# Performance work log

Hardware: AMD Instinct MI355X
Metric: run time of the kernel (lower is better)

## Reference

```python
import jax, jax.numpy as jnp
import numpy as np

BETA = 0.25

def setup_inputs() -> dict:
    key = jax.random.key(0)
    k1, k2 = jax.random.split(key)
    z = jax.random.normal(k1, (8, 4096, 256), dtype=jnp.float32)
    emb = jax.random.normal(k2, (8192, 256), dtype=jnp.float32) * (1.0 / 8192.0)
    code_age = jnp.zeros((8192,), dtype=jnp.float32)
    code_usage = jnp.zeros((8192,), dtype=jnp.float32)
    return {"z": z, "emb": emb, "code_age": code_age, "code_usage": code_usage}

def reference(z, emb, code_age, code_usage):
    e_dim = emb.shape[-1]
    z_flat = z.reshape(-1, e_dim)  # [M, d]
    # squared euclidean distance (same argmin as torch.cdist)
    z2 = jnp.sum(z_flat * z_flat, axis=-1, keepdims=True)          # [M, 1]
    e2 = jnp.sum(emb * emb, axis=-1)[None, :]                       # [1, n_e]
    dist = z2 - 2.0 * jnp.einsum('md,nd->mn', z_flat, emb) + e2     # [M, n_e]
    idx = jnp.argmin(dist, axis=1)                                  # [M]
    z_q = emb[idx].reshape(z.shape)                                 # gather
    # losses (forward values; stop_gradients irrelevant for fwd)
    diff2 = (z_q - z) ** 2
    loss_commit = BETA * jnp.mean(diff2)   # beta * mean((sg(z_q) - z)^2)
    loss_codebook = jnp.mean(diff2)        # mean((z_q - sg(z))^2)
    # straight-through output: z + sg(z_q - z) == z_q numerically
    z_q_out = z + jax.lax.stop_gradient(z_q - z)
    # code stats update: age += 1 then age[idx] = 0; usage.index_add(idx, 1)
    new_code_age = (code_age + 1.0).at[idx].set(0.0)
    new_code_usage = code_usage.at[idx].add(jnp.ones_like(idx, dtype=code_usage.dtype))
    return (z_q_out, loss_commit, loss_codebook, idx, new_code_age, new_code_usage)
```

## Files before the change

### kernel.cpp

```cpp
#include <hip/hip_runtime.h>
#include <stdint.h>

typedef unsigned int u32;
typedef unsigned long long u64;
typedef _Float16 half8 __attribute__((ext_vector_type(8)));
typedef _Float16 half4 __attribute__((ext_vector_type(4)));
typedef float f32x4 __attribute__((ext_vector_type(4)));

#define M_TOT 32768
#define D_DIM 256
#define N_E   8192
#define BM 128
#define BN 256
#define SA 264
#define SB 40
#define MARGIN_RAW 0.16384f
#define CAND_MARGIN2_RAW 0.35f
#define CBUF 2048

__device__ __forceinline__ u64 umax64(u64 a, u64 b) { return a > b ? a : b; }

__device__ __forceinline__ u32 map_f32(float f) {
    u32 u = __float_as_uint(f);
    return u ^ ((u32)((int)u >> 31) | 0x80000000u);
}

__device__ void exact_pair(const float* __restrict__ z, const float* __restrict__ emb,
                           int m, int n, u64* __restrict__ bg)
{
    #pragma clang fp contract(off)
    const float* zp = z + (long)m * D_DIM;
    const float* ep = emb + (long)n * D_DIM;
    float z2 = 0.0f;
    for (int h = 0; h < 2; ++h) {
        const float* p = zp + h * 128;
        float r0 = p[0]*p[0], r1 = p[1]*p[1], r2 = p[2]*p[2], r3 = p[3]*p[3];
        float r4 = p[4]*p[4], r5 = p[5]*p[5], r6 = p[6]*p[6], r7 = p[7]*p[7];
        for (int k = 8; k < 128; k += 8) {
            r0 += p[k+0]*p[k+0]; r1 += p[k+1]*p[k+1];
            r2 += p[k+2]*p[k+2]; r3 += p[k+3]*p[k+3];
            r4 += p[k+4]*p[k+4]; r5 += p[k+5]*p[k+5];
            r6 += p[k+6]*p[k+6]; r7 += p[k+7]*p[k+7];
        }
        z2 = z2 + (((r0 + r1) + (r2 + r3)) + ((r4 + r5) + (r6 + r7)));
    }
    float v0 = 0.f, v1 = 0.f, v2 = 0.f, v3 = 0.f;
    for (int it = 0; it < 16; ++it) {
        const float* zz = zp + it * 16;
        const float* ee = ep + it * 16;
        v0 = zz[0]*ee[0] + (zz[4]*ee[4] + (zz[8]*ee[8] + (zz[12]*ee[12] + v0)));
        v1 = zz[1]*ee[1] + (zz[5]*ee[5] + (zz[9]*ee[9] + (zz[13]*ee[13] + v1)));
        v2 = zz[2]*ee[2] + (zz[6]*ee[6] + (zz[10]*ee[10] + (zz[14]*ee[14] + v2)));
        v3 = zz[3]*ee[3] + (zz[7]*ee[7] + (zz[11]*ee[11] + (zz[15]*ee[15] + v3)));
    }
    float dot = (v0 + v1) + (v2 + v3);
    float q = z2 - 2.0f * dot;
    atomicMin(&bg[m], ((u64)map_f32(q) << 32) | (u64)(u32)n);
}

__global__ void k_setup(const float* __restrict__ emb, _Float16* __restrict__ emb_h,
                        int* counts, int* amb_cnt, u64* bg) {
    long i = (long)blockIdx.x * 1024 + threadIdx.x * 4;
    float4 v = *(const float4*)(emb + i);
    half4 h = { (_Float16)(v.x * 8192.0f), (_Float16)(v.y * 8192.0f),
                (_Float16)(v.z * 8192.0f), (_Float16)(v.w * 8192.0f) };
    *(half4*)(emb_h + i) = h;

    int gid = blockIdx.x * 256 + threadIdx.x;
    if (gid < M_TOT) bg[gid] = ~0ull;
    if (gid < N_E) counts[gid] = 0;
    if (gid == 0) *amb_cnt = 0;
}

__global__ __launch_bounds__(512, 2) void k_argmax(
    const float* __restrict__ z, const _Float16* __restrict__ emb_h,
    int* __restrict__ idx_int,
    int* __restrict__ amb_list, int* __restrict__ amb_cnt, float* __restrict__ smax)
{
    __shared__ _Float16 smem[4 * 16384];

    const int t = threadIdx.x;
    const int w = t >> 6;
    const int wrow = w >> 1;
    const int wcol = w & 1;
    const int lane = t & 63;
    const int quad = lane >> 4;
    const int l15 = lane & 15;
    const int m0 = blockIdx.x * BM;
    const int wn = wcol * 128;

    const int nbase = t >> 3;
    const int kgr = (t & 7) ^ (nbase & 7);

    auto stage = [&](int s) {
        const int nt2 = s >> 2, kb2 = s & 3;
        const _Float16* gb = emb_h + (long)nt2 * (BN * D_DIM) + kb2 * 64 + kgr * 8;
        _Float16* lbase = smem + (s & 3) * 16384 + t * 8;
        #pragma unroll
        for (int i = 0; i < 4; ++i) {
            __builtin_amdgcn_global_load_lds(
                (const __attribute__((address_space(1))) u32*)(gb + (long)(nbase + i * 64) * D_DIM),
                (__attribute__((address_space(3))) u32*)(lbase + i * 4096), 16, 0, 0);
        }
    };

    #pragma unroll
    for (int i = 0; i < 16; ++i) {
        int c = i * 512 + t;
        int row = c >> 6, q4 = c & 63;
        float4 v = *(const float4*)&z[(long)(m0 + row) * D_DIM + q4 * 4];
        half4 h = { (_Float16)v.x, (_Float16)v.y, (_Float16)v.z, (_Float16)v.w };
        *(half4*)((char*)smem + (((row << 9) + (q4 << 3)) ^ ((row & 7) << 4))) = h;
    }
    __syncthreads();

    half8 afl[2][8];
    #pragma unroll
    for (int mi = 0; mi < 2; ++mi) {
        #pragma unroll
        for (int ks = 0; ks < 8; ++ks) {
            const int row = wrow * 32 + mi * 16 + l15;
            afl[mi][ks] = *(const half8*)((const char*)smem +
                    (((row << 9) + (ks << 6) + (quad << 4)) ^ ((row & 7) << 4)));
        }
    }
    __syncthreads();
    stage(0); stage(1); stage(2);

    float f1[8], f2[8];
    u32 pay[8];
    #pragma unroll
    for (int g = 0; g < 8; ++g) { f1[g] = -3.0e38f; f2[g] = -3.0e38f; pay[g] = 0u; }

    for (int nt = 0; nt < N_E / BN; ++nt) {
        f32x4 acc[2][8];
        #pragma unroll
        for (int mi = 0; mi < 2; ++mi)
            #pragma unroll
            for (int ni = 0; ni < 8; ++ni)
                acc[mi][ni] = (f32x4){0.f, 0.f, 0.f, 0.f};

        #pragma unroll
        for (int kb = 0; kb < 4; ++kb) {
            const int s = nt * 4 + kb;
            asm volatile("s_waitcnt vmcnt(8)" ::: "memory");
            __builtin_amdgcn_s_barrier();
            __builtin_amdgcn_sched_barrier(0);
            stage((s + 3) & 127);
            const int bufoff = (s & 3) * 32768;
            #pragma unroll
            for (int kk = 0; kk < 2; ++kk) {
                half8 bf[8];
                #pragma unroll
                for (int ni = 0; ni < 8; ++ni) {
                    const int n = wn + ni * 16 + l15;
                    bf[ni] = *(const half8*)((const char*)smem + bufoff +
                            (n << 7) + (((kk << 6) + (quad << 4)) ^ ((n & 7) << 4)));
                }
                __builtin_amdgcn_s_setprio(1);
                #pragma unroll
                for (int mi = 0; mi < 2; ++mi)
                    #pragma unroll
                    for (int ni = 0; ni < 8; ++ni)
                        acc[mi][ni] = __builtin_amdgcn_mfma_f32_16x16x32_f16(
                            afl[mi][kb * 2 + kk], bf[ni], acc[mi][ni], 0, 0, 0);
                __builtin_amdgcn_s_setprio(0);
            }
        }

        const u32 pbase = (u32)(nt << 3);
        #pragma unroll
        for (int mi = 0; mi < 2; ++mi) {
            #pragma unroll
            for (int reg = 0; reg < 4; ++reg) {
                const int g = mi * 4 + reg;
                float s0 = acc[mi][0][reg], s1 = acc[mi][1][reg];
                float s2 = acc[mi][2][reg], s3 = acc[mi][3][reg];
                float s4 = acc[mi][4][reg], s5 = acc[mi][5][reg];
                float s6 = acc[mi][6][reg], s7 = acc[mi][7][reg];
                float h01 = fmaxf(s0, s1), l01 = fminf(s0, s1);
                float h23 = fmaxf(s2, s3), l23 = fminf(s2, s3);
                float h45 = fmaxf(s4, s5), l45 = fminf(s4, s5);
                float h67 = fmaxf(s6, s7), l67 = fminf(s6, s7);
                u32 j01 = (s1 > s0) ? 1u : 0u;
                u32 j23 = (s3 > s2) ? 3u : 2u;
                u32 j45 = (s5 > s4) ? 5u : 4u;
                u32 j67 = (s7 > s6) ? 7u : 6u;
                float hA = fmaxf(h01, h23);
                float sA = fmaxf(fminf(h01, h23), fmaxf(l01, l23));
                u32 jA = (h23 > h01) ? j23 : j01;
                float hB = fmaxf(h45, h67);
                float sB = fmaxf(fminf(h45, h67), fmaxf(l45, l67));
                u32 jB = (h67 > h45) ? j67 : j45;
                float m8 = fmaxf(hA, hB);
                float sec8 = fmaxf(fminf(hA, hB), fmaxf(sA, sB));
                u32 j8 = (hB > hA) ? jB : jA;
                bool rec = m8 > f1[g];
                f2[g] = fmaxf(f2[g], fmaxf(sec8, fminf(f1[g], m8)));
                f1[g] = fmaxf(f1[g], m8);
                pay[g] = rec ? (pbase | j8) : pay[g];
            }
        }
    }

    __syncthreads();
    u64* redB1   = (u64*)smem;
    float* redF1 = (float*)((char*)smem + 2048);
    float* redF2 = (float*)((char*)smem + 3072);

    #pragma unroll
    for (int g = 0; g < 8; ++g) {
        u32 nt_ = pay[g] >> 3, j_ = pay[g] & 7u;
        u32 n = nt_ * 256 + (u32)wn + j_ * 16 + (u32)l15;
        u64 B = ((u64)map_f32(f1[g]) << 32) | (u64)(8191u - n);
        float F1 = f1[g], F2 = f2[g];
        #pragma unroll
        for (int o = 1; o < 16; o <<= 1) {
            float oF1 = __shfl_xor(F1, o, 64);
            float oF2 = __shfl_xor(F2, o, 64);
            u64 oB = __shfl_xor(B, o, 64);
            F2 = fmaxf(fmaxf(F2, oF2), fminf(F1, oF1));
            F1 = fmaxf(F1, oF1);
            B = umax64(B, oB);
        }
        if (l15 == 0) {
            int mi = g >> 2, reg = g & 3;
            int r = mi * 16 + quad * 4 + reg;
            redB1[w * 32 + r] = B;
            redF1[w * 32 + r] = F1;
            redF2[w * 32 + r] = F2;
        }
    }
    __syncthreads();
    if (t < BM) {
        const int wr = t >> 5;
        const int r  = t & 31;
        u64 B = 0ull; float F1 = -3.0e38f, F2 = -3.0e38f;
        #pragma unroll
        for (int wc = 0; wc < 2; ++wc) {
            int wi = wr * 2 + wc;
            u64 v = redB1[wi * 32 + r];
            float nf1 = redF1[wi * 32 + r], nf2 = redF2[wi * 32 + r];
            F2 = fmaxf(fmaxf(F2, nf2), fminf(F1, nf1));
            F1 = fmaxf(F1, nf1);
            B = umax64(B, v);
        }
        int m = m0 + t;
        idx_int[m] = 8191 - (int)(B & 0xFFFFFFFFu);
        smax[m] = F1;
        if (F1 - F2 < MARGIN_RAW) {
            int p = atomicAdd(amb_cnt, 1);
            if (p < M_TOT) amb_list[p] = m;
        }
    }
}

__global__ __launch_bounds__(256, 2) void k_cand(
    const float* __restrict__ z, const float* __restrict__ emb,
    const _Float16* __restrict__ emb_h, const float* __restrict__ smax,
    const int* __restrict__ amb_list, const int* __restrict__ amb_cnt,
    u64* __restrict__ bg)
{
    __shared__ _Float16 As[64 * SA];
    __shared__ _Float16 Bs[BN * SB];
    __shared__ int ml[64];
    __shared__ float thr_s[64];
    __shared__ u32 cbuf[CBUF];
    __shared__ int ccnt;

    int cnt = *amb_cnt; if (cnt > M_TOT) cnt = M_TOT;
    const int ngroups = (cnt + 63) >> 6;
    const int nunits = ngroups * 8;
    const int t = threadIdx.x;
    const int w = t >> 6, lane = t & 63, quad = lane >> 4, l15 = lane & 15;
    const int wn = w * 64;
    if (t == 0) ccnt = 0;

    for (int u = blockIdx.x; u < nunits; u += gridDim.x) {
        const int g = u >> 3, slice = u & 7;
        __syncthreads();
        if (t < 64) {
            int gi = g * 64 + t;
            int mm = amb_list[gi < cnt ? gi : cnt - 1];
            ml[t] = mm;
            thr_s[t] = smax[mm] - CAND_MARGIN2_RAW;
        }
        __syncthreads();
        #pragma unroll
        for (int i = 0; i < 16; ++i) {
            int c = i * 256 + t;
            int row = c >> 6, q = c & 63;
            float4 v = *(const float4*)&z[(long)ml[row] * D_DIM + q * 4];
            half4 h = { (_Float16)v.x, (_Float16)v.y, (_Float16)v.z, (_Float16)v.w };
            *(half4*)&As[row * SA + q * 4] = h;
        }
        __syncthreads();

        for (int st = 0; st < 4; ++st) {
            const int n0 = slice * 1024 + st * 256;
            f32x4 acc[4][4];
            #pragma unroll
            for (int mi = 0; mi < 4; ++mi)
                #pragma unroll
                for (int ni = 0; ni < 4; ++ni)
                    acc[mi][ni] = (f32x4){0.f, 0.f, 0.f, 0.f};

            for (int ks = 0; ks < 8; ++ks) {
                __syncthreads();
                #pragma unroll
                for (int i = 0; i < 4; ++i) {
                    int c = i * 256 + t;
                    int col = c >> 2, seg = c & 3;
                    *(half8*)&Bs[col * SB + seg * 8] =
                        *(const half8*)&emb_h[(long)(n0 + col) * D_DIM + ks * 32 + seg * 8];
                }
                __syncthreads();
                half8 af[4], bf[4];
                #pragma unroll
                for (int mi = 0; mi < 4; ++mi)
                    af[mi] = *(const half8*)&As[(mi * 16 + l15) * SA + ks * 32 + quad * 8];
                #pragma unroll
                for (int ni = 0; ni < 4; ++ni)
                    bf[ni] = *(const half8*)&Bs[(wn + ni * 16 + l15) * SB + quad * 8];
                #pragma unroll
                for (int mi = 0; mi < 4; ++mi)
                    #pragma unroll
                    for (int ni = 0; ni < 4; ++ni)
                        acc[mi][ni] = __builtin_amdgcn_mfma_f32_16x16x32_f16(af[mi], bf[ni], acc[mi][ni], 0, 0, 0);
            }

            #pragma unroll
            for (int mi = 0; mi < 4; ++mi) {
                #pragma unroll
                for (int reg = 0; reg < 4; ++reg) {
                    int r = mi * 16 + quad * 4 + reg;
                    float th = thr_s[r];
                    u32 mm = (u32)ml[r];
                    #pragma unroll
                    for (int ni = 0; ni < 4; ++ni) {
                        if (acc[mi][ni][reg] >= th) {
                            u32 n = (u32)(n0 + wn + ni * 16 + l15);
                            int p = atomicAdd(&ccnt, 1);
                            if (p < CBUF) cbuf[p] = (mm << 13) | n;
                            else exact_pair(z, emb, (int)mm, (int)n, bg);
                        }
                    }
                }
            }
        }

        __syncthreads();
        int nc = ccnt; if (nc > CBUF) nc = CBUF;
        for (int j = t; j < nc; j += 256) {
            u32 cd = cbuf[j];
            exact_pair(z, emb, (int)(cd >> 13), (int)(cd & 8191u), bg);
        }
        __syncthreads();
        if (t == 0) ccnt = 0;
    }
}

__global__ __launch_bounds__(256) void k_out(
    const float* __restrict__ z, const float* __restrict__ emb,
    const int* __restrict__ idx_int, const u64* __restrict__ bg,
    float* __restrict__ zq, float* __restrict__ out_idx_f,
    double* __restrict__ accum_part, int* __restrict__ counts)
{
    const int b = blockIdx.x, t = threadIdx.x;
    int gid = b * 256 + t;
    if (gid < M_TOT) {
        u64 bv = bg[gid];
        int ic = (bv != ~0ull) ? (int)(bv & 8191u) : idx_int[gid];
        out_idx_f[gid] = (float)ic;
        atomicAdd(&counts[ic], 1);
    }

    float s = 0.f;
    #pragma unroll
    for (int i = 0; i < 8; ++i) {
        long base = ((long)(b * 8 + i) * 256 + t) * 4;
        int m = (int)(base >> 8), d = (int)(base & 255);
        u64 bm = bg[m];
        int idxm = (bm != ~0ull) ? (int)(bm & 8191u) : idx_int[m];
        float4 ev = *(const float4*)&emb[(long)idxm * D_DIM + d];
        float4 zv = *(const float4*)&z[base];
        *(float4*)&zq[base] = ev;
        float dx = ev.x - zv.x, dy = ev.y - zv.y;
        float dz2 = ev.z - zv.z, dw = ev.w - zv.w;
        s += dx * dx + dy * dy + dz2 * dz2 + dw * dw;
    }
    for (int o = 32; o > 0; o >>= 1) s += __shfl_down(s, o, 64);
    __shared__ float red[4];
    if ((t & 63) == 0) red[t >> 6] = s;
    __syncthreads();
    if (t == 0) accum_part[b] = (double)(red[0] + red[1] + red[2] + red[3]);
}

__global__ void k_final(const float* __restrict__ code_age, const float* __restrict__ code_usage,
                        const int* __restrict__ counts, const double* __restrict__ accum_part,
                        float* __restrict__ out_losses, float* __restrict__ out_age,
                        float* __restrict__ out_usage)
{
    int n = blockIdx.x * 256 + threadIdx.x;
    if (n < N_E) {
        int c = counts[n];
        out_age[n] = (c > 0) ? 0.0f : code_age[n] + 1.0f;
        out_usage[n] = code_usage[n] + (float)c;
    }
    if (blockIdx.x == 0) {
        const int t = threadIdx.x;
        __shared__ double dred[256];
        dred[t] = accum_part[t] + accum_part[t + 256]
                + accum_part[t + 512] + accum_part[t + 768];
        __syncthreads();
        for (int o = 128; o > 0; o >>= 1) {
            if (t < o) dred[t] += dred[t + o];
            __syncthreads();
        }
        if (t == 0) {
            double mean = dred[0] / (double)((long)M_TOT * D_DIM);
            out_losses[0] = (float)(0.25 * mean);
            out_losses[1] = (float)mean;
        }
    }
}

extern "C" void kernel_launch(void* const* d_in, const int* in_sizes, int n_in,
                              void* d_out, int out_size, void* d_ws, size_t ws_size,
                              hipStream_t stream) {
    const float* z          = (const float*)d_in[0];
    const float* emb        = (const float*)d_in[1];
    const float* code_age   = (const float*)d_in[2];
    const float* code_usage = (const float*)d_in[3];

    float* out        = (float*)d_out;
    float* out_zq     = out;
    float* out_losses = out + 8388608;
    float* out_idx    = out + 8388610;
    float* out_age    = out + 8388610 + M_TOT;
    float* out_usage  = out_age + N_E;

    char* ws = (char*)d_ws;
    _Float16* emb_h = (_Float16*)(ws);
    int* idx_int    = (int*)(ws + 4194304);
    int* counts     = (int*)(ws + 4325376);
    int* amb_list   = (int*)(ws + 4358144);
    int* amb_cnt    = (int*)(ws + 4489216);
    u64* bg         = (u64*)(ws + 4489232);
    float* smax     = (float*)(ws + 4751376);
    double* accum_part = (double*)(ws + 4882448);

    k_setup<<<2048, 256, 0, stream>>>(emb, emb_h, counts, amb_cnt, bg);
    k_argmax<<<M_TOT / BM, 512, 0, stream>>>(z, emb_h, idx_int,
                                             amb_list, amb_cnt, smax);
    k_cand<<<512, 256, 0, stream>>>(z, emb, emb_h, smax, amb_list, amb_cnt, bg);
    k_out<<<1024, 256, 0, stream>>>(z, emb, idx_int, bg, out_zq, out_idx,
                                    accum_part, counts);
    k_final<<<32, 256, 0, stream>>>(code_age, code_usage, counts, accum_part,
                                    out_losses, out_age, out_usage);
}
```

Before: 338.8 us.

## Split argmax codebook range across two blocks and merge partial maxima

Each argmax block now scans only half the codebook, doubling the grid so more blocks run concurrently per CU. Shared memory staging drops from four to two buffers with full vmcnt waits, lowering LDS use to allow two resident blocks. A new merge kernel combines per-half best/second-best scores, writes indices, and builds the ambiguous-row list. Costs include reloading z per half, a shallower prefetch pipeline, and an extra kernel launch with workspace traffic.

```diff
diff --git a/kernel.cpp b/kernel.cpp
--- a/kernel.cpp
+++ b/kernel.cpp
@@ -74,10 +74,9 @@
 
 __global__ __launch_bounds__(512, 2) void k_argmax(
     const float* __restrict__ z, const _Float16* __restrict__ emb_h,
-    int* __restrict__ idx_int,
-    int* __restrict__ amb_list, int* __restrict__ amb_cnt, float* __restrict__ smax)
-{
-    __shared__ _Float16 smem[4 * 16384];
+    u64* __restrict__ wsB, float* __restrict__ wsF2)
+{
+    __shared__ _Float16 smem[2 * 16384];
 
     const int t = threadIdx.x;
     const int w = t >> 6;
@@ -86,16 +85,18 @@
     const int lane = t & 63;
     const int quad = lane >> 4;
     const int l15 = lane & 15;
-    const int m0 = blockIdx.x * BM;
+    const int qtr = blockIdx.x & 1;
+    const int m0 = (blockIdx.x >> 1) * BM;
     const int wn = wcol * 128;
+    const int NT0 = qtr * 16;
 
     const int nbase = t >> 3;
     const int kgr = (t & 7) ^ (nbase & 7);
 
     auto stage = [&](int s) {
-        const int nt2 = s >> 2, kb2 = s & 3;
+        const int nt2 = NT0 + (s >> 2), kb2 = s & 3;
         const _Float16* gb = emb_h + (long)nt2 * (BN * D_DIM) + kb2 * 64 + kgr * 8;
-        _Float16* lbase = smem + (s & 3) * 16384 + t * 8;
+        _Float16* lbase = smem + (s & 1) * 16384 + t * 8;
         #pragma unroll
         for (int i = 0; i < 4; ++i) {
             __builtin_amdgcn_global_load_lds(
@@ -125,14 +126,14 @@
         }
     }
     __syncthreads();
-    stage(0); stage(1); stage(2);
+    stage(0);
 
     float f1[8], f2[8];
     u32 pay[8];
     #pragma unroll
     for (int g = 0; g < 8; ++g) { f1[g] = -3.0e38f; f2[g] = -3.0e38f; pay[g] = 0u; }
 
-    for (int nt = 0; nt < N_E / BN; ++nt) {
+    for (int nt = NT0; nt < NT0 + 16; ++nt) {
         f32x4 acc[2][8];
         #pragma unroll
         for (int mi = 0; mi < 2; ++mi)
@@ -142,12 +143,12 @@
 
         #pragma unroll
         for (int kb = 0; kb < 4; ++kb) {
-            const int s = nt * 4 + kb;
-            asm volatile("s_waitcnt vmcnt(8)" ::: "memory");
+            const int s = (nt - NT0) * 4 + kb;
+            asm volatile("s_waitcnt vmcnt(0)" ::: "memory");
             __builtin_amdgcn_s_barrier();
             __builtin_amdgcn_sched_barrier(0);
-            stage((s + 3) & 127);
-            const int bufoff = (s & 3) * 32768;
+            if (s + 1 < 64) stage(s + 1);
+            const int bufoff = (s & 1) * 32768;
             #pragma unroll
             for (int kk = 0; kk < 2; ++kk) {
                 half8 bf[8];
@@ -245,13 +246,33 @@
             F1 = fmaxf(F1, nf1);
             B = umax64(B, v);
         }
-        int m = m0 + t;
-        idx_int[m] = 8191 - (int)(B & 0xFFFFFFFFu);
-        smax[m] = F1;
-        if (F1 - F2 < MARGIN_RAW) {
-            int p = atomicAdd(amb_cnt, 1);
-            if (p < M_TOT) amb_list[p] = m;
-        }
+        wsB[qtr * M_TOT + m0 + t] = B;
+        wsF2[qtr * M_TOT + m0 + t] = F2;
+    }
+}
+
+__global__ void k_merge(const u64* __restrict__ wsB, const float* __restrict__ wsF2,
+                        int* __restrict__ idx_int, float* __restrict__ smax,
+                        int* __restrict__ amb_list, int* __restrict__ amb_cnt)
+{
+    int m = blockIdx.x * 256 + threadIdx.x;
+    u64 B = 0ull; float F1 = -3.0e38f, F2 = -3.0e38f;
+    #pragma unroll
+    for (int q = 0; q < 2; ++q) {
+        u64 b = wsB[q * M_TOT + m];
+        u32 v = (u32)(b >> 32);
+        u32 u = v ^ ((u32)((int)(~v) >> 31) | 0x80000000u);
+        float nf1 = __uint_as_float(u);
+        float nf2 = wsF2[q * M_TOT + m];
+        F2 = fmaxf(fmaxf(F2, nf2), fminf(F1, nf1));
+        F1 = fmaxf(F1, nf1);
+        B = umax64(B, b);
+    }
+    idx_int[m] = 8191 - (int)(B & 0xFFFFFFFFu);
+    smax[m] = F1;
+    if (F1 - F2 < MARGIN_RAW) {
+        int p = atomicAdd(amb_cnt, 1);
+        if (p < M_TOT) amb_list[p] = m;
     }
 }
 
@@ -449,10 +470,13 @@
     u64* bg         = (u64*)(ws + 4489232);
     float* smax     = (float*)(ws + 4751376);
     double* accum_part = (double*)(ws + 4882448);
+    u64* wsB        = (u64*)(ws + 4890640);
+    float* wsF2     = (float*)(ws + 5414928);
 
     k_setup<<<2048, 256, 0, stream>>>(emb, emb_h, counts, amb_cnt, bg);
-    k_argmax<<<M_TOT / BM, 512, 0, stream>>>(z, emb_h, idx_int,
-                                             amb_list, amb_cnt, smax);
+    k_argmax<<<2 * (M_TOT / BM), 512, 0, stream>>>(z, emb_h, wsB, wsF2);
+    k_merge<<<M_TOT / 256, 256, 0, stream>>>(wsB, wsF2, idx_int, smax,
+                                             amb_list, amb_cnt);
     k_cand<<<512, 256, 0, stream>>>(z, emb, emb_h, smax, amb_list, amb_cnt, bg);
     k_out<<<1024, 256, 0, stream>>>(z, emb, idx_int, bg, out_zq, out_idx,
                                     accum_part, counts);
```

New measurement: 349.8 us. +3.3%, slower.

## Restructure candidate-rescoring GEMM with async double-buffered LDS loads and register-held A

Applied to the files above, without the earlier changes.

The candidate kernel now uses 512 threads and 128-row groups, holding the A fragments in registers for the whole K range. The B tiles are streamed into XOR-swizzled LDS through double-buffered global_load_lds with one barrier per stage, replacing the synchronous copy that needed two barriers per k-step. It also raises MFMA priority with setprio. This is meant to hide global-load latency and avoid LDS bank conflicts in the ambiguous-row rescoring pass. In exchange, register pressure goes up, and rows are padded to 128 per group, which can waste work when the ambiguous count is small.

```diff
diff --git a/kernel.cpp b/kernel.cpp
--- a/kernel.cpp
+++ b/kernel.cpp
@@ -12,8 +12,6 @@
 #define N_E   8192
 #define BM 128
 #define BN 256
-#define SA 264
-#define SB 40
 #define MARGIN_RAW 0.16384f
 #define CAND_MARGIN2_RAW 0.35f
 #define CBUF 2048
@@ -255,91 +253,130 @@
     }
 }
 
-__global__ __launch_bounds__(256, 2) void k_cand(
+__global__ __launch_bounds__(512, 2) void k_cand(
     const float* __restrict__ z, const float* __restrict__ emb,
     const _Float16* __restrict__ emb_h, const float* __restrict__ smax,
     const int* __restrict__ amb_list, const int* __restrict__ amb_cnt,
     u64* __restrict__ bg)
 {
-    __shared__ _Float16 As[64 * SA];
-    __shared__ _Float16 Bs[BN * SB];
-    __shared__ int ml[64];
-    __shared__ float thr_s[64];
+    __shared__ _Float16 smem[2 * 16384];
+    __shared__ int ml[128];
+    __shared__ float thr_s[128];
     __shared__ u32 cbuf[CBUF];
     __shared__ int ccnt;
 
     int cnt = *amb_cnt; if (cnt > M_TOT) cnt = M_TOT;
-    const int ngroups = (cnt + 63) >> 6;
+    const int ngroups = (cnt + 127) >> 7;
     const int nunits = ngroups * 8;
+
     const int t = threadIdx.x;
-    const int w = t >> 6, lane = t & 63, quad = lane >> 4, l15 = lane & 15;
-    const int wn = w * 64;
+    const int w = t >> 6;
+    const int wrow = w >> 1;
+    const int wcol = w & 1;
+    const int lane = t & 63;
+    const int quad = lane >> 4;
+    const int l15 = lane & 15;
+    const int wn = wcol * 128;
+
+    const int nbase = t >> 3;
+    const int kgr = (t & 7) ^ (nbase & 7);
+
     if (t == 0) ccnt = 0;
 
     for (int u = blockIdx.x; u < nunits; u += gridDim.x) {
         const int g = u >> 3, slice = u & 7;
         __syncthreads();
-        if (t < 64) {
-            int gi = g * 64 + t;
+        if (t < 128) {
+            int gi = g * 128 + t;
             int mm = amb_list[gi < cnt ? gi : cnt - 1];
             ml[t] = mm;
             thr_s[t] = smax[mm] - CAND_MARGIN2_RAW;
         }
         __syncthreads();
+
         #pragma unroll
         for (int i = 0; i < 16; ++i) {
-            int c = i * 256 + t;
-            int row = c >> 6, q = c & 63;
-            float4 v = *(const float4*)&z[(long)ml[row] * D_DIM + q * 4];
+            int c = i * 512 + t;
+            int row = c >> 6, q4 = c & 63;
+            float4 v = *(const float4*)&z[(long)ml[row] * D_DIM + q4 * 4];
             half4 h = { (_Float16)v.x, (_Float16)v.y, (_Float16)v.z, (_Float16)v.w };
-            *(half4*)&As[row * SA + q * 4] = h;
-        }
-        __syncthreads();
-
-        for (int st = 0; st < 4; ++st) {
-            const int n0 = slice * 1024 + st * 256;
-            f32x4 acc[4][4];
-            #pragma unroll
-            for (int mi = 0; mi < 4; ++mi)
+            *(half4*)((char*)smem + (((row << 9) + (q4 << 3)) ^ ((row & 7) << 4))) = h;
+        }
+        __syncthreads();
+
+        half8 afl[2][8];
+        #pragma unroll
+        for (int mi = 0; mi < 2; ++mi) {
+            #pragma unroll
+            for (int ks = 0; ks < 8; ++ks) {
+                const int row = wrow * 32 + mi * 16 + l15;
+                afl[mi][ks] = *(const half8*)((const char*)smem +
+                        (((row << 9) + (ks << 6) + (quad << 4)) ^ ((row & 7) << 4)));
+            }
+        }
+        __syncthreads();
+
+        auto stage = [&](int s) {
+            const int nt2 = slice * 4 + (s >> 2), kb2 = s & 3;
+            const _Float16* gb = emb_h + (long)nt2 * (BN * D_DIM) + kb2 * 64 + kgr * 8;
+            _Float16* lbase = smem + (s & 1) * 16384 + t * 8;
+            #pragma unroll
+            for (int i = 0; i < 4; ++i) {
+                __builtin_amdgcn_global_load_lds(
+                    (const __attribute__((address_space(1))) u32*)(gb + (long)(nbase + i * 64) * D_DIM),
+                    (__attribute__((address_space(3))) u32*)(lbase + i * 4096), 16, 0, 0);
+            }
+        };
+        stage(0);
+
+        for (int ntl = 0; ntl < 4; ++ntl) {
+            f32x4 acc[2][8];
+            #pragma unroll
+            for (int mi = 0; mi < 2; ++mi)
                 #pragma unroll
-                for (int ni = 0; ni < 4; ++ni)
+                for (int ni = 0; ni < 8; ++ni)
                     acc[mi][ni] = (f32x4){0.f, 0.f, 0.f, 0.f};
 
-            for (int ks = 0; ks < 8; ++ks) {
-                __syncthreads();
+            #pragma unroll
+            for (int kb = 0; kb < 4; ++kb) {
+                const int s = ntl * 4 + kb;
+                asm volatile("s_waitcnt vmcnt(0)" ::: "memory");
+                __builtin_amdgcn_s_barrier();
+                __builtin_amdgcn_sched_barrier(0);
+                if (s + 1 < 16) stage(s + 1);
+                const int bufoff = (s & 1) * 32768;
                 #pragma unroll
-                for (int i = 0; i < 4; ++i) {
-                    int c = i * 256 + t;
-                    int col = c >> 2, seg = c & 3;
-                    *(half8*)&Bs[col * SB + seg * 8] =
-                        *(const half8*)&emb_h[(long)(n0 + col) * D_DIM + ks * 32 + seg * 8];
+                for (int kk = 0; kk < 2; ++kk) {
+                    half8 bf[8];
+                    #pragma unroll
+                    for (int ni = 0; ni < 8; ++ni) {
+                        const int n = wn + ni * 16 + l15;
+                        bf[ni] = *(const half8*)((const char*)smem + bufoff +
+                                (n << 7) + (((kk << 6) + (quad << 4)) ^ ((n & 7) << 4)));
+                    }
+                    __builtin_amdgcn_s_setprio(1);
+                    #pragma unroll
+                    for (int mi = 0; mi < 2; ++mi)
+                        #pragma unroll
+                        for (int ni = 0; ni < 8; ++ni)
+                            acc[mi][ni] = __builtin_amdgcn_mfma_f32_16x16x32_f16(
+                                afl[mi][kb * 2 + kk], bf[ni], acc[mi][ni], 0, 0, 0);
+                    __builtin_amdgcn_s_setprio(0);
                 }
-                __syncthreads();
-                half8 af[4], bf[4];
-                #pragma unroll
-                for (int mi = 0; mi < 4; ++mi)
-                    af[mi] = *(const half8*)&As[(mi * 16 + l15) * SA + ks * 32 + quad * 8];
-                #pragma unroll
-                for (int ni = 0; ni < 4; ++ni)
-                    bf[ni] = *(const half8*)&Bs[(wn + ni * 16 + l15) * SB + quad * 8];
-                #pragma unroll
-                for (int mi = 0; mi < 4; ++mi)
-                    #pragma unroll
-                    for (int ni = 0; ni < 4; ++ni)
-                        acc[mi][ni] = __builtin_amdgcn_mfma_f32_16x16x32_f16(af[mi], bf[ni], acc[mi][ni], 0, 0, 0);
-            }
-
-            #pragma unroll
-            for (int mi = 0; mi < 4; ++mi) {
+            }
+
+            const int gn0 = slice * 1024 + ntl * 256;
+            #pragma unroll
+            for (int mi = 0; mi < 2; ++mi) {
                 #pragma unroll
                 for (int reg = 0; reg < 4; ++reg) {
-                    int r = mi * 16 + quad * 4 + reg;
+                    const int r = wrow * 32 + mi * 16 + quad * 4 + reg;
                     float th = thr_s[r];
                     u32 mm = (u32)ml[r];
                     #pragma unroll
-                    for (int ni = 0; ni < 4; ++ni) {
+                    for (int ni = 0; ni < 8; ++ni) {
                         if (acc[mi][ni][reg] >= th) {
-                            u32 n = (u32)(n0 + wn + ni * 16 + l15);
+                            u32 n = (u32)(gn0 + wn + ni * 16 + l15);
                             int p = atomicAdd(&ccnt, 1);
                             if (p < CBUF) cbuf[p] = (mm << 13) | n;
                             else exact_pair(z, emb, (int)mm, (int)n, bg);
@@ -351,7 +388,7 @@
 
         __syncthreads();
         int nc = ccnt; if (nc > CBUF) nc = CBUF;
-        for (int j = t; j < nc; j += 256) {
+        for (int j = t; j < nc; j += 512) {
             u32 cd = cbuf[j];
             exact_pair(z, emb, (int)(cd >> 13), (int)(cd & 8191u), bg);
         }
@@ -453,7 +490,7 @@
     k_setup<<<2048, 256, 0, stream>>>(emb, emb_h, counts, amb_cnt, bg);
     k_argmax<<<M_TOT / BM, 512, 0, stream>>>(z, emb_h, idx_int,
                                              amb_list, amb_cnt, smax);
-    k_cand<<<512, 256, 0, stream>>>(z, emb, emb_h, smax, amb_list, amb_cnt, bg);
+    k_cand<<<512, 512, 0, stream>>>(z, emb, emb_h, smax, amb_list, amb_cnt, bg);
     k_out<<<1024, 256, 0, stream>>>(z, emb, idx_int, bg, out_zq, out_idx,
                                     accum_part, counts);
     k_final<<<32, 256, 0, stream>>>(code_age, code_usage, counts, accum_part,
```

After: 437.1 us. 29.0% more time.
